# Kernel optimization log

Hardware: AMD Instinct MI355X
Metric: run time of the kernel (lower is better)

## Reference

```python
import jax, jax.numpy as jnp
import numpy as np

B, T, V = 16, 2048, 512


def setup_inputs() -> dict:
    key = jax.random.key(0)
    k1, k2, k3, k4 = jax.random.split(key, 4)
    idx = jax.random.randint(k1, (B, T), 0, V)
    # torch init: normal(mean=0.1, std=0.02)
    pos_table = 0.1 + 0.02 * jax.random.normal(k2, (T, 1), dtype=jnp.float32)
    Wq = 0.1 + 0.02 * jax.random.normal(k3, (V, V), dtype=jnp.float32)
    Wv = 0.1 + 0.02 * jax.random.normal(k4, (V, V), dtype=jnp.float32)
    return {"idx": idx, "pos_table": pos_table, "Wq": Wq, "Wv": Wv}


def reference(idx, pos_table, Wq, Wv):
    # e = one_hot token embedding: (B, T, V)
    e = jax.nn.one_hot(idx, Wq.shape[0], dtype=pos_table.dtype)
    t = idx.shape[1]
    # relative positions, clamped at 0 (pos[pos<0]=0 in torch)
    pos = jnp.arange(t)
    rel = jnp.maximum(pos[:, None] - pos[None, :], 0)  # (T, T) int
    pe = pos_table[rel, 0]  # (T, T)
    causal = jnp.tril(jnp.ones((t, t), dtype=bool))
    # layer one (Wk falsy branch): einsum('BTe,Tt->BTt', e, pe).tril() @ e
    a1 = jnp.where(causal, jnp.einsum('btv,ts->bts', e, pe), 0.0)  # (B,T,T)
    l1 = a1 @ e  # (B, T, V)
    # layer two (Wk truthy branch; note Wk weight is never applied in fwd):
    # (Wq(e) @ l1^T).tril() @ Wv(e)
    Q = e @ Wq.T   # (B, T, V)
    Vv = e @ Wv.T  # (B, T, V)
    a2 = jnp.where(causal, jnp.einsum('btv,bsv->bts', Q, l1), 0.0)  # (B,T,T)
    logits = a2 @ Vv  # (B, T, V)
    return logits
```

## Files before the change

### kernel.cpp

```cpp
#include <hip/hip_runtime.h>
#include <hip/hip_bf16.h>
#include <math.h>

#define BB 16
#define TT 2048
#define VV 512

typedef __attribute__((ext_vector_type(8))) short short8;
typedef __attribute__((ext_vector_type(4))) float floatx4;

static __device__ inline ushort f2bf(float f) {
  __hip_bfloat16 h = __float2bfloat16(f);
  return *(ushort*)&h;
}

static __device__ __forceinline__ void cp16(const void* g, void* l) {
  __builtin_amdgcn_global_load_lds((const __attribute__((address_space(1))) void*)g,
                                   (__attribute__((address_space(3))) void*)l, 16, 0, 0);
}

static __device__ __forceinline__ void balance_map(int y, int z, int* t_t, int* b) {
  const int r = y & 3, q = z >> 2;
  int t = (q == 0) ? r : (q == 1) ? (r + 8) : (q == 2) ? (7 - r) : (15 - r);
  *t_t = t;
  *b = ((z & 3) << 2) | (y >> 2);
}


__global__ __launch_bounds__(256) void k_transpose_wq(const float* __restrict__ Wq,
                                                      ushort* __restrict__ WqT) {
  int u = blockIdx.x;
  for (int v = threadIdx.x; v < VV; v += blockDim.x)
    WqT[u * VV + v] = f2bf(Wq[(size_t)v * VV + u]);
}

__global__ __launch_bounds__(256) void k_build_pe(const float* __restrict__ h,
                                                  ushort* __restrict__ PE) {
  int t = blockIdx.x;
  ushort* out = PE + (size_t)t * TT;
  for (int p = threadIdx.x; p < TT; p += blockDim.x)
    out[p] = (p <= t) ? f2bf(h[t - p]) : (ushort)0;
}

__global__ __launch_bounds__(256) void k_build_mv(const int* __restrict__ idx,
                                                  const float* __restrict__ Wv,
                                                  const ushort* __restrict__ WqT,
                                                  ushort* __restrict__ M,
                                                  ushort* __restrict__ VvT) {
  int bv = blockIdx.x;
  int b = bv >> 9, v = bv & (VV - 1);
  __shared__ float wrow[VV];
  __shared__ ushort qrow[VV];
  for (int u = threadIdx.x; u < VV; u += blockDim.x) {
    wrow[u] = Wv[(size_t)v * VV + u];
    qrow[u] = WqT[(size_t)v * VV + u];
  }
  __syncthreads();
  const int* row = idx + b * TT;
  ushort* om = M + (size_t)bv * TT;
  ushort* ov = VvT + (size_t)bv * TT;
  for (int s4 = threadIdx.x * 4; s4 < TT; s4 += blockDim.x * 4) {
    int4 iv = *(const int4*)(row + s4);
    ushort4 m, w;
    m.x = qrow[iv.x];  w.x = f2bf(wrow[iv.x]);
    m.y = qrow[iv.y];  w.y = f2bf(wrow[iv.y]);
    m.z = qrow[iv.z];  w.z = f2bf(wrow[iv.z]);
    m.w = qrow[iv.w];  w.w = f2bf(wrow[iv.w]);
    *(ushort4*)(om + s4) = m;
    *(ushort4*)(ov + s4) = w;
  }
}


#define GEMM_PRELUDE()                                                         \
  __shared__ __attribute__((aligned(16))) short As[2 * 128 * 32];              \
  __shared__ __attribute__((aligned(16))) short Bs[2 * 128 * 32];              \
  const int tid = threadIdx.x;                                                 \
  const int lane = tid & 63;                                                   \
  const int wm = (tid >> 6) & 1, wn = tid >> 7;                                \
  const int quad = lane >> 4, ln = lane & 15;                                  \
  const int rr = tid >> 2;                                                     \
  const int cg = (((tid & 3) ^ (rr & 3)) << 3);                                \
  short* a_dst = &As[tid * 8];                                                 \
  short* b_dst = &Bs[tid * 8];                                                 \
  const short* ap[4];                                                          \
  const short* bp[4];                                                          \
  _Pragma("unroll") for (int i = 0; i < 4; i++)                                \
      ap[i] = &As[(wm * 64 + i * 16 + ln) * 32 + ((quad ^ (ln & 3)) << 3)];    \
  _Pragma("unroll") for (int j = 0; j < 4; j++)                                \
      bp[j] = &Bs[(wn * 64 + j * 16 + ln) * 32 + ((quad ^ (ln & 3)) << 3)];

#define GEMM_STAGE(c, PA0, PA1, PB0, PB1)                                      \
  {                                                                            \
    const int _o = (c) << 12;                    \
    cp16((PA0), a_dst + _o);                                                   \
    cp16((PA1), a_dst + _o + 2048);                                            \
    cp16((PB0), b_dst + _o);                                                   \
    cp16((PB1), b_dst + _o + 2048);                                            \
  }

#define GEMM_COMPUTE(c)                                                        \
  {                                                                            \
    const int _o = (c) << 12;                                                  \
    short8 af[4], bfr[4];                                                      \
    _Pragma("unroll") for (int i = 0; i < 4; i++)                              \
        af[i] = *(const short8*)(ap[i] + _o);                                  \
    _Pragma("unroll") for (int j = 0; j < 4; j++)                              \
        bfr[j] = *(const short8*)(bp[j] + _o);                                 \
    _Pragma("unroll") for (int i = 0; i < 4; i++)                              \
        _Pragma("unroll") for (int j = 0; j < 4; j++)                          \
            acc[i][j] = __builtin_amdgcn_mfma_f32_16x16x32_bf16(               \
                af[i], bfr[j], acc[i][j], 0, 0, 0);                            \
  }

#define ZERO_ACC()                                                             \
  _Pragma("unroll") for (int i = 0; i < 4; i++)                                \
      _Pragma("unroll") for (int j = 0; j < 4; j++)                            \
          acc[i][j] = (floatx4){0.f, 0.f, 0.f, 0.f};

__global__ __launch_bounds__(256) void k_gemm_gt(const ushort* __restrict__ M,
                                                 const ushort* __restrict__ PE,
                                                 ushort* __restrict__ GT) {
  int s_t, b;
  balance_map(blockIdx.y, blockIdx.z, &s_t, &b);
  const int u_t = blockIdx.x;
  const int u0 = u_t << 7, s0 = s_t << 7;
  const int nk = (s_t << 2) + 4;
  GEMM_PRELUDE();
  const ushort* a_src0 = M + ((size_t)((b << 9) + u0 + rr)) * TT + cg;
  const ushort* a_src1 = a_src0 + (size_t)64 * TT;
  const ushort* b_src0 = PE + (size_t)(s0 + rr) * TT + cg;
  const ushort* b_src1 = b_src0 + (size_t)64 * TT;
  floatx4 acc[4][4];
  ZERO_ACC();
  GEMM_STAGE(0, a_src0, a_src1, b_src0, b_src1);
  __syncthreads();
  int cur = 0;
#pragma unroll 1
  for (int kt = 0; kt < nk; ++kt) {
    if (kt + 1 < nk) {
      const int ko = (kt + 1) << 5;
      GEMM_STAGE(cur ^ 1, a_src0 + ko, a_src1 + ko, b_src0 + ko, b_src1 + ko);
    }
    GEMM_COMPUTE(cur);
    __syncthreads();
    cur ^= 1;
  }
#pragma unroll
  for (int i = 0; i < 4; i++)
#pragma unroll
    for (int j = 0; j < 4; j++) {
      const int rowb = u0 + wm * 64 + i * 16 + quad * 4;
      const int col = s0 + wn * 64 + j * 16 + ln;
#pragma unroll
      for (int r = 0; r < 4; r++)
        GT[((size_t)((b << 9) + rowb + r)) * TT + col] = f2bf(acc[i][j][r]);
    }
}

__global__ __launch_bounds__(256) void k_diag(const int* __restrict__ idx,
                                              const ushort* __restrict__ GT,
                                              ushort* __restrict__ a2d) {
  const int t_t = blockIdx.x, b = blockIdx.y;
  const int t0 = t_t << 7;
  ushort* outt = a2d + (((size_t)(b << 4) + t_t) << 14);
  for (int e = threadIdx.x; e < 2048; e += 256) {
    const int r = e >> 4;
    const int c8 = (e & 15) << 3;
    const int u = idx[(b << 11) + t0 + r];
    const ushort* src = GT + ((size_t)((b << 9) + u)) * TT + t0 + c8;
    ushort4 lo = *(const ushort4*)(src);
    ushort4 hi = *(const ushort4*)(src + 4);
    ushort vals[8] = {lo.x, lo.y, lo.z, lo.w, hi.x, hi.y, hi.z, hi.w};
    ushort o[8];
#pragma unroll
    for (int k = 0; k < 8; ++k) o[k] = (c8 + k <= r) ? vals[k] : (ushort)0;
    *(ushort4*)(outt + r * 128 + c8) = *(ushort4*)&o[0];
    *(ushort4*)(outt + r * 128 + c8 + 4) = *(ushort4*)&o[4];
  }
}

__global__ __launch_bounds__(256) void k_gemm2(const int* __restrict__ idx,
                                               const ushort* __restrict__ GT,
                                               const ushort* __restrict__ a2d,
                                               const ushort* __restrict__ VvT,
                                               float* __restrict__ out) {
  int t_t, b;
  balance_map(blockIdx.y, blockIdx.z, &t_t, &b);
  const int j_t = blockIdx.x;
  const int t0 = t_t << 7, j0 = j_t << 7;
  const int nk_main = t_t << 2;
  const int nk = nk_main + 4;
  GEMM_PRELUDE();
  const int u0 = idx[(b << 11) + t0 + rr];
  const int u1 = idx[(b << 11) + t0 + rr + 64];
  const ushort* a_src0 = GT + ((size_t)(b << 9) + u0) * TT + cg;
  const ushort* a_src1 = GT + ((size_t)(b << 9) + u1) * TT + cg;
  const ushort* b_src0 = VvT + ((size_t)((b << 9) + j0 + rr)) * TT + cg;
  const ushort* b_src1 = b_src0 + (size_t)64 * TT;
  const ushort* ad0 = a2d + (((size_t)(b << 4) + t_t) << 14) + (size_t)rr * 128 + cg;
  const ushort* ad1 = ad0 + (size_t)64 * 128;
#define A0_AT(kt) ((kt) < nk_main ? a_src0 + ((kt) << 5) : ad0 + (((kt) - nk_main) << 5))
#define A1_AT(kt) ((kt) < nk_main ? a_src1 + ((kt) << 5) : ad1 + (((kt) - nk_main) << 5))
  floatx4 acc[4][4];
  ZERO_ACC();
  GEMM_STAGE(0, A0_AT(0), A1_AT(0), b_src0, b_src1);
  __syncthreads();
  int cur = 0;
#pragma unroll 1
  for (int kt = 0; kt < nk; ++kt) {
    if (kt + 1 < nk) {
      const int ko = (kt + 1) << 5;
      GEMM_STAGE(cur ^ 1, A0_AT(kt + 1), A1_AT(kt + 1), b_src0 + ko, b_src1 + ko);
    }
    GEMM_COMPUTE(cur);
    __syncthreads();
    cur ^= 1;
  }
#undef A0_AT
#undef A1_AT
#pragma unroll
  for (int i = 0; i < 4; i++)
#pragma unroll
    for (int j = 0; j < 4; j++) {
      const int rowb = t0 + wm * 64 + i * 16 + quad * 4;
      const int col = j0 + wn * 64 + j * 16 + ln;
#pragma unroll
      for (int r = 0; r < 4; r++)
        out[((size_t)((b << 11) + rowb + r)) * VV + col] = acc[i][j][r];
    }
}

extern "C" void kernel_launch(void* const* d_in, const int* in_sizes, int n_in,
                              void* d_out, int out_size, void* d_ws, size_t ws_size,
                              hipStream_t stream) {
  const int* idx = (const int*)d_in[0];
  const float* pos_table = (const float*)d_in[1];
  const float* Wq = (const float*)d_in[2];
  const float* Wv = (const float*)d_in[3];
  float* out = (float*)d_out;

  char* ws = (char*)d_ws;
  ushort* WqT = (ushort*)(ws);
  ushort* PE = (ushort*)(ws + 524288UL);
  ushort* M = (ushort*)(ws + 8912896UL);
  ushort* VvT = (ushort*)(ws + 42467328UL);
  ushort* GT = (ushort*)(ws + 76021760UL);
  ushort* a2d = (ushort*)(ws + 109576192UL);

  k_transpose_wq<<<dim3(VV), 256, 0, stream>>>(Wq, WqT);
  k_build_pe<<<dim3(TT), 256, 0, stream>>>(pos_table, PE);
  k_build_mv<<<dim3(BB * VV), 256, 0, stream>>>(idx, Wv, WqT, M, VvT);
  k_gemm_gt<<<dim3(4, 16, BB), 256, 0, stream>>>(M, PE, GT);
  k_diag<<<dim3(16, BB), 256, 0, stream>>>(idx, GT, a2d);
  k_gemm2<<<dim3(4, 16, BB), 256, 0, stream>>>(idx, GT, a2d, VvT, out);
}
```

Measured before the change: 225.6 us.

## Fuse prep kernels, mask diagonal in-register, and remap GEMM tiles across XCDs

Merges the Wq transpose and PE build into one launch, and drops the separate diagonal-masking kernel by applying the causal mask to A fragments inside gemm2's last K tiles. Both GEMMs move to a 1D grid with a band_map that spreads batches across the 8 XCDs and orders tiles from heavy to light. build_mv stores Wv as bf16 in shared memory and writes 8 elements per thread with a new block ordering. This removes launches and an intermediate buffer, at the cost of per-element masking work in the diagonal tiles.

```diff
diff --git a/kernel.cpp b/kernel.cpp
--- a/kernel.cpp
+++ b/kernel.cpp
@@ -19,27 +19,30 @@
                                    (__attribute__((address_space(3))) void*)l, 16, 0, 0);
 }
 
-static __device__ __forceinline__ void balance_map(int y, int z, int* t_t, int* b) {
-  const int r = y & 3, q = z >> 2;
-  int t = (q == 0) ? r : (q == 1) ? (r + 8) : (q == 2) ? (7 - r) : (15 - r);
-  *t_t = t;
-  *b = ((z & 3) << 2) | (y >> 2);
-}
-
-
-__global__ __launch_bounds__(256) void k_transpose_wq(const float* __restrict__ Wq,
-                                                      ushort* __restrict__ WqT) {
-  int u = blockIdx.x;
-  for (int v = threadIdx.x; v < VV; v += blockDim.x)
-    WqT[u * VV + v] = f2bf(Wq[(size_t)v * VV + u]);
-}
-
-__global__ __launch_bounds__(256) void k_build_pe(const float* __restrict__ h,
-                                                  ushort* __restrict__ PE) {
-  int t = blockIdx.x;
-  ushort* out = PE + (size_t)t * TT;
-  for (int p = threadIdx.x; p < TT; p += blockDim.x)
-    out[p] = (p <= t) ? f2bf(h[t - p]) : (ushort)0;
+static __device__ __forceinline__ void band_map(int h, int* b, int* ct, int* tt) {
+  const int xcd = h & 7, rank = h >> 3;
+  const int band = rank >> 5, cc = rank & 31, g = cc >> 3, slot = cc & 7;
+  *b = xcd | ((slot >> 2) << 3);
+  *ct = slot & 3;
+  *tt = (band == 0) ? (15 - g) : (band == 1) ? (11 - g) : (band == 2) ? (4 + g) : g;
+}
+
+
+__global__ __launch_bounds__(256) void k_pre(const float* __restrict__ Wq,
+                                             const float* __restrict__ h,
+                                             ushort* __restrict__ WqT,
+                                             ushort* __restrict__ PE) {
+  const int blk = blockIdx.x;
+  if (blk < VV) {
+    const int u = blk;
+    for (int v = threadIdx.x; v < VV; v += blockDim.x)
+      WqT[u * VV + v] = f2bf(Wq[(size_t)v * VV + u]);
+  } else {
+    const int t = blk - VV;
+    ushort* out = PE + (size_t)t * TT;
+    for (int p = threadIdx.x; p < TT; p += blockDim.x)
+      out[p] = (p <= t) ? f2bf(h[t - p]) : (ushort)0;
+  }
 }
 
 __global__ __launch_bounds__(256) void k_build_mv(const int* __restrict__ idx,
@@ -47,28 +50,34 @@
                                                   const ushort* __restrict__ WqT,
                                                   ushort* __restrict__ M,
                                                   ushort* __restrict__ VvT) {
-  int bv = blockIdx.x;
-  int b = bv >> 9, v = bv & (VV - 1);
-  __shared__ float wrow[VV];
+  const int h = blockIdx.x;
+  const int b = (h & 7) | (((h >> 3) & 1) << 3);
+  const int v = h >> 4;
+  const int bv = (b << 9) + v;
+  __shared__ ushort wrow[VV];
   __shared__ ushort qrow[VV];
   for (int u = threadIdx.x; u < VV; u += blockDim.x) {
-    wrow[u] = Wv[(size_t)v * VV + u];
+    wrow[u] = f2bf(Wv[(size_t)v * VV + u]);
     qrow[u] = WqT[(size_t)v * VV + u];
   }
   __syncthreads();
   const int* row = idx + b * TT;
   ushort* om = M + (size_t)bv * TT;
   ushort* ov = VvT + (size_t)bv * TT;
-  for (int s4 = threadIdx.x * 4; s4 < TT; s4 += blockDim.x * 4) {
-    int4 iv = *(const int4*)(row + s4);
-    ushort4 m, w;
-    m.x = qrow[iv.x];  w.x = f2bf(wrow[iv.x]);
-    m.y = qrow[iv.y];  w.y = f2bf(wrow[iv.y]);
-    m.z = qrow[iv.z];  w.z = f2bf(wrow[iv.z]);
-    m.w = qrow[iv.w];  w.w = f2bf(wrow[iv.w]);
-    *(ushort4*)(om + s4) = m;
-    *(ushort4*)(ov + s4) = w;
-  }
+  const int s8 = threadIdx.x * 8;
+  int4 iv0 = *(const int4*)(row + s8);
+  int4 iv1 = *(const int4*)(row + s8 + 4);
+  short8 m8, w8;
+  m8[0] = qrow[iv0.x];  w8[0] = wrow[iv0.x];
+  m8[1] = qrow[iv0.y];  w8[1] = wrow[iv0.y];
+  m8[2] = qrow[iv0.z];  w8[2] = wrow[iv0.z];
+  m8[3] = qrow[iv0.w];  w8[3] = wrow[iv0.w];
+  m8[4] = qrow[iv1.x];  w8[4] = wrow[iv1.x];
+  m8[5] = qrow[iv1.y];  w8[5] = wrow[iv1.y];
+  m8[6] = qrow[iv1.z];  w8[6] = wrow[iv1.z];
+  m8[7] = qrow[iv1.w];  w8[7] = wrow[iv1.w];
+  *(short8*)(om + s8) = m8;
+  *(short8*)(ov + s8) = w8;
 }
 
 
@@ -113,6 +122,25 @@
                 af[i], bfr[j], acc[i][j], 0, 0, 0);                            \
   }
 
+#define GEMM_COMPUTE_MASKED(c, DK)                                             \
+  {                                                                            \
+    const int _o = (c) << 12;                                                  \
+    short8 af[4], bfr[4];                                                      \
+    _Pragma("unroll") for (int i = 0; i < 4; i++)                              \
+        af[i] = *(const short8*)(ap[i] + _o);                                  \
+    _Pragma("unroll") for (int j = 0; j < 4; j++)                              \
+        bfr[j] = *(const short8*)(bp[j] + _o);                                 \
+    _Pragma("unroll") for (int i = 0; i < 4; i++) {                            \
+      const int lim = (wm * 64 + i * 16 + ln) - (DK) - (quad << 3);            \
+      _Pragma("unroll") for (int e = 0; e < 8; e++)                            \
+          if (e > lim) af[i][e] = 0;                                           \
+    }                                                                          \
+    _Pragma("unroll") for (int i = 0; i < 4; i++)                              \
+        _Pragma("unroll") for (int j = 0; j < 4; j++)                          \
+            acc[i][j] = __builtin_amdgcn_mfma_f32_16x16x32_bf16(               \
+                af[i], bfr[j], acc[i][j], 0, 0, 0);                            \
+  }
+
 #define ZERO_ACC()                                                             \
   _Pragma("unroll") for (int i = 0; i < 4; i++)                                \
       _Pragma("unroll") for (int j = 0; j < 4; j++)                            \
@@ -121,9 +149,8 @@
 __global__ __launch_bounds__(256) void k_gemm_gt(const ushort* __restrict__ M,
                                                  const ushort* __restrict__ PE,
                                                  ushort* __restrict__ GT) {
-  int s_t, b;
-  balance_map(blockIdx.y, blockIdx.z, &s_t, &b);
-  const int u_t = blockIdx.x;
+  int b, u_t, s_t;
+  band_map(blockIdx.x, &b, &u_t, &s_t);
   const int u0 = u_t << 7, s0 = s_t << 7;
   const int nk = (s_t << 2) + 4;
   GEMM_PRELUDE();
@@ -158,36 +185,12 @@
     }
 }
 
-__global__ __launch_bounds__(256) void k_diag(const int* __restrict__ idx,
-                                              const ushort* __restrict__ GT,
-                                              ushort* __restrict__ a2d) {
-  const int t_t = blockIdx.x, b = blockIdx.y;
-  const int t0 = t_t << 7;
-  ushort* outt = a2d + (((size_t)(b << 4) + t_t) << 14);
-  for (int e = threadIdx.x; e < 2048; e += 256) {
-    const int r = e >> 4;
-    const int c8 = (e & 15) << 3;
-    const int u = idx[(b << 11) + t0 + r];
-    const ushort* src = GT + ((size_t)((b << 9) + u)) * TT + t0 + c8;
-    ushort4 lo = *(const ushort4*)(src);
-    ushort4 hi = *(const ushort4*)(src + 4);
-    ushort vals[8] = {lo.x, lo.y, lo.z, lo.w, hi.x, hi.y, hi.z, hi.w};
-    ushort o[8];
-#pragma unroll
-    for (int k = 0; k < 8; ++k) o[k] = (c8 + k <= r) ? vals[k] : (ushort)0;
-    *(ushort4*)(outt + r * 128 + c8) = *(ushort4*)&o[0];
-    *(ushort4*)(outt + r * 128 + c8 + 4) = *(ushort4*)&o[4];
-  }
-}
-
 __global__ __launch_bounds__(256) void k_gemm2(const int* __restrict__ idx,
                                                const ushort* __restrict__ GT,
-                                               const ushort* __restrict__ a2d,
                                                const ushort* __restrict__ VvT,
                                                float* __restrict__ out) {
-  int t_t, b;
-  balance_map(blockIdx.y, blockIdx.z, &t_t, &b);
-  const int j_t = blockIdx.x;
+  int b, j_t, t_t;
+  band_map(blockIdx.x, &b, &j_t, &t_t);
   const int t0 = t_t << 7, j0 = j_t << 7;
   const int nk_main = t_t << 2;
   const int nk = nk_main + 4;
@@ -198,27 +201,26 @@
   const ushort* a_src1 = GT + ((size_t)(b << 9) + u1) * TT + cg;
   const ushort* b_src0 = VvT + ((size_t)((b << 9) + j0 + rr)) * TT + cg;
   const ushort* b_src1 = b_src0 + (size_t)64 * TT;
-  const ushort* ad0 = a2d + (((size_t)(b << 4) + t_t) << 14) + (size_t)rr * 128 + cg;
-  const ushort* ad1 = ad0 + (size_t)64 * 128;
-#define A0_AT(kt) ((kt) < nk_main ? a_src0 + ((kt) << 5) : ad0 + (((kt) - nk_main) << 5))
-#define A1_AT(kt) ((kt) < nk_main ? a_src1 + ((kt) << 5) : ad1 + (((kt) - nk_main) << 5))
   floatx4 acc[4][4];
   ZERO_ACC();
-  GEMM_STAGE(0, A0_AT(0), A1_AT(0), b_src0, b_src1);
+  GEMM_STAGE(0, a_src0, a_src1, b_src0, b_src1);
   __syncthreads();
   int cur = 0;
 #pragma unroll 1
   for (int kt = 0; kt < nk; ++kt) {
     if (kt + 1 < nk) {
       const int ko = (kt + 1) << 5;
-      GEMM_STAGE(cur ^ 1, A0_AT(kt + 1), A1_AT(kt + 1), b_src0 + ko, b_src1 + ko);
-    }
-    GEMM_COMPUTE(cur);
+      GEMM_STAGE(cur ^ 1, a_src0 + ko, a_src1 + ko, b_src0 + ko, b_src1 + ko);
+    }
+    if (kt < nk_main) {
+      GEMM_COMPUTE(cur);
+    } else {
+      const int dk = (kt - nk_main) << 5;
+      GEMM_COMPUTE_MASKED(cur, dk);
+    }
     __syncthreads();
     cur ^= 1;
   }
-#undef A0_AT
-#undef A1_AT
 #pragma unroll
   for (int i = 0; i < 4; i++)
 #pragma unroll
@@ -246,12 +248,9 @@
   ushort* M = (ushort*)(ws + 8912896UL);
   ushort* VvT = (ushort*)(ws + 42467328UL);
   ushort* GT = (ushort*)(ws + 76021760UL);
-  ushort* a2d = (ushort*)(ws + 109576192UL);
-
-  k_transpose_wq<<<dim3(VV), 256, 0, stream>>>(Wq, WqT);
-  k_build_pe<<<dim3(TT), 256, 0, stream>>>(pos_table, PE);
+
+  k_pre<<<dim3(VV + TT), 256, 0, stream>>>(Wq, pos_table, WqT, PE);
   k_build_mv<<<dim3(BB * VV), 256, 0, stream>>>(idx, Wv, WqT, M, VvT);
-  k_gemm_gt<<<dim3(4, 16, BB), 256, 0, stream>>>(M, PE, GT);
-  k_diag<<<dim3(16, BB), 256, 0, stream>>>(idx, GT, a2d);
-  k_gemm2<<<dim3(4, 16, BB), 256, 0, stream>>>(idx, GT, a2d, VvT, out);
-}
+  k_gemm_gt<<<dim3(1024), 256, 0, stream>>>(M, PE, GT);
+  k_gemm2<<<dim3(1024), 256, 0, stream>>>(idx, GT, VvT, out);
+}
```

Result: faster. 210.3 us (-6.8%).
